# Kernel tuning notes

Hardware: AMD Instinct MI355X
Metric: run time of the kernel (lower is better)

Reference implementation:

```python
import jax, jax.numpy as jnp
import numpy as np

WS = 8      # window_size
NH = 8      # n_heads
EPS = 1e-06


def _rel_coords(ws):
    # Swin-style relative position index table, matches torch buffer construction
    c = np.stack(np.meshgrid(np.arange(ws), np.arange(ws), indexing='ij'))  # [2,ws,ws]
    c = c.reshape(2, -1)                      # [2, L]
    rel = c[:, :, None] - c[:, None, :]       # [2, L, L]
    rel = rel.transpose(1, 2, 0) + (ws - 1)   # [L, L, 2]
    rel[:, :, 0] *= 2 * ws - 1
    return jnp.asarray(rel.sum(-1), dtype=jnp.int32)  # [L, L]


def rms_film(x, t, gw, bw):
    # x: [B,C,H,W], t: [B,d_t]; RMS over channel dim, FiLM scale/shift from t
    g = (t @ gw.T)[:, :, None, None]
    b = (t @ bw.T)[:, :, None, None]
    return g * x * jax.lax.rsqrt(jnp.mean(x * x, axis=1, keepdims=True) + EPS) + b


def window_attn(x, wq, wk, wv, wo_w, wo_b, rpb):
    B, C, H, W = x.shape
    h, w = H // WS, W // WS
    L = WS * WS
    dh = C // NH
    # partition into windows: [B, h, w, L, C]
    xw = x.reshape(B, C, h, WS, w, WS).transpose(0, 2, 4, 3, 5, 1).reshape(B, h, w, L, C)

    def heads(p):
        y = xw @ p.T  # Linear, no bias
        return y.reshape(B, h, w, L, NH, dh).transpose(0, 1, 2, 4, 3, 5)  # [B,h,w,n,L,dh]

    q, k, v = heads(wq), heads(wk), heads(wv)
    bias = rpb[:, _rel_coords(WS)]  # [NH, L, L] gather from bias table
    attn = jnp.einsum('bhwnld,bhwnmd->bhwnlm', q, k) / float(np.sqrt(dh)) + bias
    o = jnp.einsum('bhwnlm,bhwnmd->bhwnld', jax.nn.softmax(attn, axis=-1), v)
    # merge windows, channel order (n c): [B, NH*dh, H, W]
    o = o.reshape(B, h, w, NH, WS, WS, dh).transpose(0, 3, 6, 1, 4, 2, 5).reshape(B, C, H, W)
    # 1x1 conv output projection (with bias)
    return jnp.einsum('bchw,oc->bohw', o, wo_w) + wo_b[None, :, None, None]


def convnext(x, t, dw_w, dw_b, gw, bw, w1, b1, w2, b2):
    # 7x7 depthwise conv, pad 3
    y = jax.lax.conv_general_dilated(
        x, dw_w, window_strides=(1, 1), padding=[(3, 3), (3, 3)],
        dimension_numbers=('NCHW', 'OIHW', 'NCHW'), feature_group_count=x.shape[1])
    y = y + dw_b[None, :, None, None]
    y = rms_film(y, t, gw, bw).transpose(0, 2, 3, 1)  # -> NHWC
    y = jax.nn.gelu(y @ w1.T + b1, approximate=False) @ w2.T + b2
    return y.transpose(0, 3, 1, 2)


def setup_inputs() -> dict:
    key = jax.random.key(0)
    ks = jax.random.split(key, 16)
    D, DT, B, H, W = 256, 256, 8, 128, 128
    DH = 4 * D
    n = lambda k, s: jax.random.normal(k, s, jnp.float32) * 0.02
    return dict(
        x=jax.random.normal(ks[0], (B, D, H, W), jnp.float32),
        t=jax.random.normal(ks[1], (B, DT), jnp.float32),
        an_g=n(ks[2], (D, DT)), an_b=n(ks[3], (D, DT)),
        wq=n(ks[4], (D, D)), wk=n(ks[5], (D, D)), wv=n(ks[6], (D, D)),
        wo_w=n(ks[7], (D, D)), wo_b=jnp.zeros((D,), jnp.float32),
        rpb=n(ks[8], (NH, (2 * WS - 1) ** 2)),
        dw_w=n(ks[9], (D, 1, 7, 7)), dw_b=jnp.zeros((D,), jnp.float32),
        fn_g=n(ks[10], (D, DT)), fn_b=n(ks[11], (D, DT)),
        w1=n(ks[12], (DH, D)), b1=jnp.zeros((DH,), jnp.float32),
        w2=n(ks[13], (D, DH)), b2=jnp.zeros((D,), jnp.float32))


def reference(x, t, an_g, an_b, wq, wk, wv, wo_w, wo_b, rpb,
              dw_w, dw_b, fn_g, fn_b, w1, b1, w2, b2):
    x = x + window_attn(rms_film(x, t, an_g, an_b), wq, wk, wv, wo_w, wo_b, rpb)
    return x + convnext(x, t, dw_w, dw_b, fn_g, fn_b, w1, b1, w2, b2)
```

## Files before the change

### kernel.cpp

```cpp
#include <hip/hip_runtime.h>
#include <math.h>

typedef __attribute__((ext_vector_type(8))) short bf16x8_t;
typedef __attribute__((ext_vector_type(4))) float f32x4;

__device__ __forceinline__ unsigned short f2bf(float f) {
  unsigned int u = __builtin_bit_cast(unsigned int, f);
  u += 0x7FFFu + ((u >> 16) & 1u);
  return (unsigned short)(u >> 16);
}
__device__ __forceinline__ float bf2f(unsigned short h) {
  unsigned int u = ((unsigned int)h) << 16;
  return __builtin_bit_cast(float, u);
}

typedef const __attribute__((address_space(1))) void* as1cv;
typedef __attribute__((address_space(3))) void* as3v;

__device__ __forceinline__ void gld_lds16(const unsigned short* g, unsigned short* l) {
  __builtin_amdgcn_global_load_lds((as1cv)g, (as3v)l, 16, 0, 0);
}

__global__ __launch_bounds__(256) void tvec_kernel(const float* __restrict__ t,
    const float* __restrict__ an_g, const float* __restrict__ an_b,
    const float* __restrict__ fn_g, const float* __restrict__ fn_b,
    float* __restrict__ gvec) {
  int d = threadIdx.x;
  int b = blockIdx.x;
  int m = blockIdx.y;
  __shared__ float ts[256];
  ts[d] = t[b * 256 + d];
  __syncthreads();
  const float* W = (m == 0) ? an_g : (m == 1) ? an_b : (m == 2) ? fn_g : fn_b;
  float acc = 0.f;
  #pragma unroll 8
  for (int k = 0; k < 256; ++k) acc += ts[k] * W[d * 256 + k];
  gvec[(m * 8 + b) * 256 + d] = acc;
}

__global__ __launch_bounds__(256) void wconv_kernel(const float* __restrict__ wq,
    const float* __restrict__ wk, const float* __restrict__ wv, const float* __restrict__ wo,
    const float* __restrict__ w1, const float* __restrict__ w2,
    unsigned short* __restrict__ outp) {
  int i = blockIdx.x * 256 + threadIdx.x;
  const float* src; int off;
  if      (i <  65536) { src = wq; off = 0; }
  else if (i < 131072) { src = wk; off = 65536; }
  else if (i < 196608) { src = wv; off = 131072; }
  else if (i < 262144) { src = wo; off = 196608; }
  else if (i < 524288) { src = w1; off = 262144; }
  else                 { src = w2; off = 524288; }
  outp[i] = f2bf(src[i - off]);
}

template<int IS_BF>
__global__ __launch_bounds__(256) void film_kernel(const void* __restrict__ in_,
    const float* __restrict__ gvec, int gsel, unsigned short* __restrict__ outbf) {
  const float* inf = (const float*)in_;
  const unsigned short* inb = (const unsigned short*)in_;
  int blk = blockIdx.x;
  int b = blk >> 8;
  int p0 = (blk & 255) << 6;
  int lane = threadIdx.x & 63;
  int cg = threadIdx.x >> 6;
  __shared__ unsigned short vals[64][264];
  __shared__ float ssred[4][64];
  __shared__ float rinvs[64];
  size_t base = ((size_t)b << 22) + p0;
  float ss = 0.f;
  #pragma unroll 4
  for (int ci = 0; ci < 64; ++ci) {
    int c = (cg << 6) + ci;
    size_t idx = base + ((size_t)c << 14) + lane;
    float v = IS_BF ? bf2f(inb[idx]) : inf[idx];
    ss += v * v;
    vals[lane][c] = f2bf(v);
  }
  ssred[cg][lane] = ss;
  __syncthreads();
  if (threadIdx.x < 64) {
    float s = ssred[0][threadIdx.x] + ssred[1][threadIdx.x] + ssred[2][threadIdx.x] + ssred[3][threadIdx.x];
    rinvs[threadIdx.x] = rsqrtf(s * (1.0f / 256.0f) + 1e-6f);
  }
  __syncthreads();
  int pix = threadIdx.x >> 2;
  int c0 = (threadIdx.x & 3) << 6;
  float rv = rinvs[pix];
  const float* gp = gvec + ((gsel * 2 + 0) * 8 + b) * 256;
  const float* bp = gvec + ((gsel * 2 + 1) * 8 + b) * 256;
  unsigned short* orow = outbf + (((size_t)b << 14) + p0 + pix) * 256 + c0;
  #pragma unroll
  for (int ch = 0; ch < 8; ++ch) {
    bf16x8_t pack;
    #pragma unroll
    for (int e = 0; e < 8; ++e) {
      int c = c0 + ch * 8 + e;
      float v = bf2f(vals[pix][c]);
      float o = gp[c] * v * rv + bp[c];
      pack[e] = (short)f2bf(o);
    }
    *(bf16x8_t*)(orow + ch * 8) = pack;
  }
}

template<int DO_GELU>
__global__ __launch_bounds__(256) void gemm_kernel(const unsigned short* __restrict__ A,
    const unsigned short* __restrict__ Bw, const float* __restrict__ bias,
    unsigned short* __restrict__ outp, int K, int N) {
  __shared__ unsigned short As[128 * 64];
  __shared__ unsigned short Bs[128 * 64];
  int tid = threadIdx.x;
  int m0 = blockIdx.x << 7;
  int n0 = blockIdx.y << 7;
  int w = tid >> 6, lane = tid & 63;
  int wm = (w >> 1) << 6, wn = (w & 1) << 6;
  f32x4 acc[4][4];
  #pragma unroll
  for (int mi = 0; mi < 4; ++mi)
    #pragma unroll
    for (int ni = 0; ni < 4; ++ni)
      acc[mi][ni] = (f32x4){0.f, 0.f, 0.f, 0.f};

  for (int k0 = 0; k0 < K; k0 += 64) {
    #pragma unroll
    for (int r2 = 0; r2 < 4; ++r2) {
      int linear = (r2 << 8) + tid;
      int row = linear >> 3;
      int ch = linear & 7;
      gld_lds16(A  + (size_t)(m0 + row) * K + k0 + ch * 8, As + linear * 8);
      gld_lds16(Bw + (size_t)(n0 + row) * K + k0 + ch * 8, Bs + linear * 8);
    }
    __syncthreads();
    #pragma unroll
    for (int kk = 0; kk < 64; kk += 32) {
      bf16x8_t af[4], bq[4];
      int lr = lane & 15;
      int lk = ((lane >> 4) << 3) + kk;
      #pragma unroll
      for (int mi = 0; mi < 4; ++mi)
        af[mi] = *(const bf16x8_t*)(As + ((wm + (mi << 4) + lr) << 6) + lk);
      #pragma unroll
      for (int ni = 0; ni < 4; ++ni)
        bq[ni] = *(const bf16x8_t*)(Bs + ((wn + (ni << 4) + lr) << 6) + lk);
      #pragma unroll
      for (int mi = 0; mi < 4; ++mi)
        #pragma unroll
        for (int ni = 0; ni < 4; ++ni)
          acc[mi][ni] = __builtin_amdgcn_mfma_f32_16x16x32_bf16(af[mi], bq[ni], acc[mi][ni], 0, 0, 0);
    }
    __syncthreads();
  }
  int lr = lane & 15, lg = lane >> 4;
  #pragma unroll
  for (int mi = 0; mi < 4; ++mi) {
    #pragma unroll
    for (int ni = 0; ni < 4; ++ni) {
      int col = n0 + wn + (ni << 4) + lr;
      int row = m0 + wm + (mi << 4) + (lg << 2);
      f32x4 a = acc[mi][ni];
      #pragma unroll
      for (int i = 0; i < 4; ++i) {
        float v = a[i];
        if (DO_GELU) {
          v += bias[col];
          v = 0.5f * v * (1.0f + erff(v * 0.70710678118654752f));
        }
        outp[(size_t)(row + i) * N + col] = f2bf(v);
      }
    }
  }
}

__global__ __launch_bounds__(256) void gemm2f_kernel(const unsigned short* __restrict__ A,
    const unsigned short* __restrict__ Bw, const float* __restrict__ bias,
    const unsigned short* __restrict__ x1, float* __restrict__ outp, int m_base) {
  __shared__ unsigned short smem[16384];
  unsigned short* As = smem;
  unsigned short* Bs = smem + 8192;
  const int K = 1024, N = 256;
  int tid = threadIdx.x;
  int m0 = blockIdx.x << 7;
  int n0 = blockIdx.y << 7;
  int w = tid >> 6, lane = tid & 63;
  int wm = (w >> 1) << 6, wn = (w & 1) << 6;
  f32x4 acc[4][4];
  #pragma unroll
  for (int mi = 0; mi < 4; ++mi)
    #pragma unroll
    for (int ni = 0; ni < 4; ++ni)
      acc[mi][ni] = (f32x4){0.f, 0.f, 0.f, 0.f};

  for (int k0 = 0; k0 < K; k0 += 64) {
    #pragma unroll
    for (int r2 = 0; r2 < 4; ++r2) {
      int linear = (r2 << 8) + tid;
      int row = linear >> 3;
      int ch = linear & 7;
      gld_lds16(A  + (size_t)(m0 + row) * K + k0 + ch * 8, As + linear * 8);
      gld_lds16(Bw + (size_t)(n0 + row) * K + k0 + ch * 8, Bs + linear * 8);
    }
    __syncthreads();
    #pragma unroll
    for (int kk = 0; kk < 64; kk += 32) {
      bf16x8_t af[4], bq[4];
      int lr = lane & 15;
      int lk = ((lane >> 4) << 3) + kk;
      #pragma unroll
      for (int mi = 0; mi < 4; ++mi)
        af[mi] = *(const bf16x8_t*)(As + ((wm + (mi << 4) + lr) << 6) + lk);
      #pragma unroll
      for (int ni = 0; ni < 4; ++ni)
        bq[ni] = *(const bf16x8_t*)(Bs + ((wn + (ni << 4) + lr) << 6) + lk);
      #pragma unroll
      for (int mi = 0; mi < 4; ++mi)
        #pragma unroll
        for (int ni = 0; ni < 4; ++ni)
          acc[mi][ni] = __builtin_amdgcn_mfma_f32_16x16x32_bf16(af[mi], bq[ni], acc[mi][ni], 0, 0, 0);
    }
    __syncthreads();
  }

  int lr = lane & 15, lg = lane >> 4;
  #pragma unroll
  for (int mi = 0; mi < 4; ++mi)
    #pragma unroll
    for (int ni = 0; ni < 4; ++ni) {
      int cl = wn + (ni << 4) + lr;
      int rl = wm + (mi << 4) + (lg << 2);
      f32x4 a = acc[mi][ni];
      #pragma unroll
      for (int i = 0; i < 4; ++i)
        smem[cl * 128 + rl + i] = f2bf(a[i]);
    }
  __syncthreads();

  int cl = tid >> 1;
  int half = tid & 1;
  int pglob0 = m_base + m0;
  int b = pglob0 >> 14;
  int pix = (pglob0 & 16383) + half * 64;
  int c = n0 + cl;
  const unsigned short* srow = smem + cl * 128 + half * 64;
  size_t gbase = ((size_t)b * 256 + c) * 16384 + pix;
  const unsigned short* xrow = x1 + gbase;
  float* orow = outp + gbase;
  float bb = bias[c];
  #pragma unroll
  for (int jj = 0; jj < 8; ++jj) {
    bf16x8_t sv = *(const bf16x8_t*)(srow + jj * 8);
    bf16x8_t xv = *(const bf16x8_t*)(xrow + jj * 8);
    #pragma unroll
    for (int e = 0; e < 8; ++e)
      orow[jj * 8 + e] = bf2f((unsigned short)sv[e]) + bf2f((unsigned short)xv[e]) + bb;
  }
}

__global__ __launch_bounds__(256) void attn_kernel(const unsigned short* __restrict__ qg,
    const unsigned short* __restrict__ kg, const unsigned short* __restrict__ vg,
    const float* __restrict__ rpb, unsigned short* __restrict__ og) {
  int wi = blockIdx.x;
  int head = blockIdx.y;
  int b = wi >> 8, wh = (wi >> 4) & 15, ww = wi & 15;
  __shared__ float qs[64][33], ks[64][33], vs[64][33];
  __shared__ float ps[64][65];
  __shared__ float rpbs[225];
  int tid = threadIdx.x;

  {
    int l = tid >> 2, quarter = tid & 3;
    size_t grow = (size_t)b * 16384 + (size_t)(wh * 8 + (l >> 3)) * 128 + ww * 8 + (l & 7);
    size_t goff = grow * 256 + head * 32 + quarter * 8;
    bf16x8_t qv = *(const bf16x8_t*)(qg + goff);
    bf16x8_t kv = *(const bf16x8_t*)(kg + goff);
    bf16x8_t vv = *(const bf16x8_t*)(vg + goff);
    #pragma unroll
    for (int e = 0; e < 8; ++e) {
      qs[l][quarter * 8 + e] = bf2f((unsigned short)qv[e]);
      ks[l][quarter * 8 + e] = bf2f((unsigned short)kv[e]);
      vs[l][quarter * 8 + e] = bf2f((unsigned short)vv[e]);
    }
  }
  if (tid < 225) rpbs[tid] = rpb[head * 225 + tid];
  __syncthreads();

  int r0 = (tid >> 4) * 4, c0 = (tid & 15) * 4;
  float s[4][4] = {};
  for (int k = 0; k < 32; ++k) {
    float qa[4], kb[4];
    #pragma unroll
    for (int i = 0; i < 4; ++i) { qa[i] = qs[r0 + i][k]; kb[i] = ks[c0 + i][k]; }
    #pragma unroll
    for (int i = 0; i < 4; ++i)
      #pragma unroll
      for (int j = 0; j < 4; ++j) s[i][j] += qa[i] * kb[j];
  }
  const float scale = 0.17677669529663689f;
  float sum[4];
  #pragma unroll
  for (int i = 0; i < 4; ++i) {
    int row = r0 + i; int il = row >> 3, jl = row & 7;
    #pragma unroll
    for (int j = 0; j < 4; ++j) {
      int col = c0 + j; int im = col >> 3, jm = col & 7;
      s[i][j] = s[i][j] * scale + rpbs[(il - im + 7) * 15 + (jl - jm + 7)];
    }
    float mx = fmaxf(fmaxf(s[i][0], s[i][1]), fmaxf(s[i][2], s[i][3]));
    mx = fmaxf(mx, __shfl_xor(mx, 1));
    mx = fmaxf(mx, __shfl_xor(mx, 2));
    mx = fmaxf(mx, __shfl_xor(mx, 4));
    mx = fmaxf(mx, __shfl_xor(mx, 8));
    float sm = 0.f;
    #pragma unroll
    for (int j = 0; j < 4; ++j) { s[i][j] = __expf(s[i][j] - mx); sm += s[i][j]; }
    sm += __shfl_xor(sm, 1);
    sm += __shfl_xor(sm, 2);
    sm += __shfl_xor(sm, 4);
    sm += __shfl_xor(sm, 8);
    sum[i] = sm;
    #pragma unroll
    for (int j = 0; j < 4; ++j) ps[row][c0 + j] = s[i][j];
  }
  __syncthreads();

  int d0 = (tid & 15) * 2;
  float o[4][2] = {};
  for (int m = 0; m < 64; ++m) {
    float pa[4], vb0 = vs[m][d0], vb1 = vs[m][d0 + 1];
    #pragma unroll
    for (int i = 0; i < 4; ++i) pa[i] = ps[r0 + i][m];
    #pragma unroll
    for (int i = 0; i < 4; ++i) { o[i][0] += pa[i] * vb0; o[i][1] += pa[i] * vb1; }
  }
  #pragma unroll
  for (int i = 0; i < 4; ++i) {
    int row = r0 + i;
    size_t orow = ((size_t)b * 16384 + (size_t)(wh * 8 + (row >> 3)) * 128 + ww * 8 + (row & 7)) * 256 + head * 32;
    float inv = 1.0f / sum[i];
    unsigned int packed = (unsigned int)f2bf(o[i][0] * inv) | ((unsigned int)f2bf(o[i][1] * inv) << 16);
    *(unsigned int*)(og + orow + d0) = packed;
  }
}

__global__ __launch_bounds__(256) void addt1_kernel(const unsigned short* __restrict__ src,
    const float* __restrict__ resid, const float* __restrict__ bias,
    unsigned short* __restrict__ outp) {
  int blk = blockIdx.x;
  int b = blk >> 8;
  int p0 = (blk & 255) << 6;
  __shared__ unsigned short vals[64][264];
  int tid = threadIdx.x;
  #pragma unroll
  for (int r = 0; r < 8; ++r) {
    int linear = r * 256 + tid;
    int row = linear >> 5;
    int ch = linear & 31;
    bf16x8_t v = *(const bf16x8_t*)(src + (((size_t)b << 14) + p0 + row) * 256 + ch * 8);
    *(bf16x8_t*)(&vals[row][ch * 8]) = v;
  }
  __syncthreads();
  int lane = tid & 63;
  int cq = tid >> 6;
  #pragma unroll 4
  for (int ci = 0; ci < 64; ++ci) {
    int c = (cq << 6) + ci;
    float v = bf2f(vals[lane][c]);
    size_t gidx = ((size_t)b << 22) + ((size_t)c << 14) + p0 + lane;
    outp[gidx] = f2bf(resid[gidx] + v + bias[c]);
  }
}

__global__ __launch_bounds__(256) void dwconv_kernel(const unsigned short* __restrict__ x1,
    const float* __restrict__ w, const float* __restrict__ bias, unsigned short* __restrict__ outp) {
  int bc = blockIdx.y;
  int c = bc & 255;
  int y0 = blockIdx.x << 6;
  __shared__ unsigned short tile[70 * 144];
  __shared__ float wf[49];
  const unsigned short* plane = x1 + ((size_t)bc << 14);
  int tid = threadIdx.x;

  for (int idx = tid; idx < 70 * 16; idx += 256) {
    int row = idx >> 4, ch = idx & 15;
    int gy = y0 - 3 + row;
    bf16x8_t v = (bf16x8_t){0, 0, 0, 0, 0, 0, 0, 0};
    if (gy >= 0 && gy < 128) v = *(const bf16x8_t*)(plane + gy * 128 + ch * 8);
    *(bf16x8_t*)(&tile[row * 144 + 8 + ch * 8]) = v;
  }
  for (int idx = tid; idx < 70 * 6; idx += 256) {
    int row = idx / 6, e = idx % 6;
    int col = (e < 3) ? (5 + e) : (133 + e);
    tile[row * 144 + col] = 0;
  }
  if (tid < 49) wf[tid] = w[c * 49 + tid];
  __syncthreads();

  int r = tid >> 2;
  int c0 = (tid & 3) << 5;
  float acc[32];
  float bb = bias[c];
  #pragma unroll
  for (int i = 0; i < 32; ++i) acc[i] = bb;

  #pragma unroll
  for (int u = 0; u < 7; ++u) {
    const unsigned short* rowp = &tile[(r + u) * 144 + c0];
    float f[48];
    #pragma unroll
    for (int k = 0; k < 6; ++k) {
      bf16x8_t v = *(const bf16x8_t*)(rowp + k * 8);
      #pragma unroll
      for (int e = 0; e < 8; ++e) f[k * 8 + e] = bf2f((unsigned short)v[e]);
    }
    #pragma unroll
    for (int t = 0; t < 7; ++t) {
      float wv = wf[u * 7 + t];
      #pragma unroll
      for (int i = 0; i < 32; ++i) acc[i] += f[i + 5 + t] * wv;
    }
  }

  unsigned short* orow = outp + ((size_t)bc << 14) + (size_t)(y0 + r) * 128 + c0;
  #pragma unroll
  for (int k = 0; k < 4; ++k) {
    bf16x8_t v;
    #pragma unroll
    for (int e = 0; e < 8; ++e) v[e] = (short)f2bf(acc[k * 8 + e]);
    *(bf16x8_t*)(orow + k * 8) = v;
  }
}

extern "C" void kernel_launch(void* const* d_in, const int* in_sizes, int n_in,
                              void* d_out, int out_size, void* d_ws, size_t ws_size,
                              hipStream_t stream) {
  const float* x    = (const float*)d_in[0];
  const float* t    = (const float*)d_in[1];
  const float* an_g = (const float*)d_in[2];
  const float* an_b = (const float*)d_in[3];
  const float* wq   = (const float*)d_in[4];
  const float* wk   = (const float*)d_in[5];
  const float* wv   = (const float*)d_in[6];
  const float* wo_w = (const float*)d_in[7];
  const float* wo_b = (const float*)d_in[8];
  const float* rpb  = (const float*)d_in[9];
  const float* dw_w = (const float*)d_in[10];
  const float* dw_b = (const float*)d_in[11];
  const float* fn_g = (const float*)d_in[12];
  const float* fn_b = (const float*)d_in[13];
  const float* w1   = (const float*)d_in[14];
  const float* b1   = (const float*)d_in[15];
  const float* w2   = (const float*)d_in[16];
  const float* b2   = (const float*)d_in[17];
  float* outp = (float*)d_out;

  char* ws = (char*)d_ws;
  const size_t MB = 1024ull * 1024ull;
  float* gvec = (float*)ws;
  unsigned short* wbf = (unsigned short*)(ws + 32768);
  unsigned short* P = (unsigned short*)(ws + 2 * MB);
  unsigned short* Q = (unsigned short*)(ws + 66 * MB);
  unsigned short* R = (unsigned short*)(ws + 130 * MB);
  unsigned short* vbuf = (unsigned short*)((char*)d_out + 64 * MB);

  unsigned short* wq_bf = wbf;
  unsigned short* wk_bf = wbf + 65536;
  unsigned short* wv_bf = wbf + 131072;
  unsigned short* wo_bf = wbf + 196608;
  unsigned short* w1_bf = wbf + 262144;
  unsigned short* w2_bf = wbf + 524288;

  tvec_kernel<<<dim3(8, 4), 256, 0, stream>>>(t, an_g, an_b, fn_g, fn_b, gvec);
  wconv_kernel<<<3072, 256, 0, stream>>>(wq, wk, wv, wo_w, w1, w2, wbf);

  film_kernel<0><<<2048, 256, 0, stream>>>(x, gvec, 0, P);

  gemm_kernel<0><<<dim3(1024, 2), 256, 0, stream>>>(P, wq_bf, nullptr, Q, 256, 256);
  gemm_kernel<0><<<dim3(1024, 2), 256, 0, stream>>>(P, wk_bf, nullptr, R, 256, 256);
  gemm_kernel<0><<<dim3(1024, 2), 256, 0, stream>>>(P, wv_bf, nullptr, vbuf, 256, 256);

  attn_kernel<<<dim3(2048, 8), 256, 0, stream>>>(Q, R, vbuf, rpb, P);

  gemm_kernel<0><<<dim3(1024, 2), 256, 0, stream>>>(P, wo_bf, nullptr, Q, 256, 256);
  addt1_kernel<<<2048, 256, 0, stream>>>(Q, x, wo_b, R);

  dwconv_kernel<<<dim3(2, 2048), 256, 0, stream>>>(R, dw_w, dw_b, Q);
  film_kernel<1><<<2048, 256, 0, stream>>>(Q, gvec, 1, P);

  for (int qtr = 0; qtr < 4; ++qtr) {
    int m_base = qtr * 32768;
    gemm_kernel<1><<<dim3(256, 8), 256, 0, stream>>>(P + (size_t)m_base * 256, w1_bf, b1, Q, 256, 1024);
    gemm2f_kernel<<<dim3(256, 2), 256, 0, stream>>>(Q, w2_bf, b2, R, outp, m_base);
  }
}
```

Measured before the change: 1.020 ms.

## Rewrite window attention with bf16 MFMA and channel-major V projection

Window attention now runs both QK^T and PV on bf16 MFMA instructions instead of scalar fp32 FMAs from LDS. Each block handles one window for all 8 heads, with each wave covering two heads. A new GEMM variant writes V transposed (channel-major) so that PV B-fragments load directly from global memory. Softmax probabilities are rounded to bf16 before the PV product, which adds a small precision loss, and the shared-memory footprint changes with a launch-bounds occupancy hint.

```diff
diff --git a/kernel.cpp b/kernel.cpp
--- a/kernel.cpp
+++ b/kernel.cpp
@@ -171,6 +171,80 @@
   }
 }
 
+__global__ __launch_bounds__(256) void gemm_t_kernel(const unsigned short* __restrict__ A,
+    const unsigned short* __restrict__ Bw, unsigned short* __restrict__ outp) {
+  __shared__ unsigned short smem[16384];
+  unsigned short* As = smem;
+  unsigned short* Bs = smem + 8192;
+  const int K = 256;
+  int tid = threadIdx.x;
+  int m0 = blockIdx.x << 7;
+  int n0 = blockIdx.y << 7;
+  int w = tid >> 6, lane = tid & 63;
+  int wm = (w >> 1) << 6, wn = (w & 1) << 6;
+  f32x4 acc[4][4];
+  #pragma unroll
+  for (int mi = 0; mi < 4; ++mi)
+    #pragma unroll
+    for (int ni = 0; ni < 4; ++ni)
+      acc[mi][ni] = (f32x4){0.f, 0.f, 0.f, 0.f};
+
+  for (int k0 = 0; k0 < K; k0 += 64) {
+    #pragma unroll
+    for (int r2 = 0; r2 < 4; ++r2) {
+      int linear = (r2 << 8) + tid;
+      int row = linear >> 3;
+      int ch = linear & 7;
+      gld_lds16(A  + (size_t)(m0 + row) * K + k0 + ch * 8, As + linear * 8);
+      gld_lds16(Bw + (size_t)(n0 + row) * K + k0 + ch * 8, Bs + linear * 8);
+    }
+    __syncthreads();
+    #pragma unroll
+    for (int kk = 0; kk < 64; kk += 32) {
+      bf16x8_t af[4], bq[4];
+      int lr = lane & 15;
+      int lk = ((lane >> 4) << 3) + kk;
+      #pragma unroll
+      for (int mi = 0; mi < 4; ++mi)
+        af[mi] = *(const bf16x8_t*)(As + ((wm + (mi << 4) + lr) << 6) + lk);
+      #pragma unroll
+      for (int ni = 0; ni < 4; ++ni)
+        bq[ni] = *(const bf16x8_t*)(Bs + ((wn + (ni << 4) + lr) << 6) + lk);
+      #pragma unroll
+      for (int mi = 0; mi < 4; ++mi)
+        #pragma unroll
+        for (int ni = 0; ni < 4; ++ni)
+          acc[mi][ni] = __builtin_amdgcn_mfma_f32_16x16x32_bf16(af[mi], bq[ni], acc[mi][ni], 0, 0, 0);
+    }
+    __syncthreads();
+  }
+
+  int lr = lane & 15, lg = lane >> 4;
+  #pragma unroll
+  for (int mi = 0; mi < 4; ++mi)
+    #pragma unroll
+    for (int ni = 0; ni < 4; ++ni) {
+      int cl = wn + (ni << 4) + lr;
+      int rl = wm + (mi << 4) + (lg << 2);
+      f32x4 a = acc[mi][ni];
+      #pragma unroll
+      for (int i = 0; i < 4; ++i)
+        smem[cl * 128 + rl + i] = f2bf(a[i]);
+    }
+  __syncthreads();
+
+  int cl = tid >> 1;
+  int half = tid & 1;
+  int b = m0 >> 14;
+  int pix = (m0 & 16383) + half * 64;
+  int c = n0 + cl;
+  const unsigned short* srow = smem + cl * 128 + half * 64;
+  unsigned short* orow = outp + ((size_t)b * 256 + c) * 16384 + pix;
+  #pragma unroll
+  for (int jj = 0; jj < 8; ++jj)
+    *(bf16x8_t*)(orow + jj * 8) = *(const bf16x8_t*)(srow + jj * 8);
+}
+
 __global__ __launch_bounds__(256) void gemm2f_kernel(const unsigned short* __restrict__ A,
     const unsigned short* __restrict__ Bw, const float* __restrict__ bias,
     const unsigned short* __restrict__ x1, float* __restrict__ outp, int m_base) {
@@ -255,89 +329,110 @@
   }
 }
 
-__global__ __launch_bounds__(256) void attn_kernel(const unsigned short* __restrict__ qg,
-    const unsigned short* __restrict__ kg, const unsigned short* __restrict__ vg,
+__global__ __launch_bounds__(256, 3) void attn_kernel(const unsigned short* __restrict__ qg,
+    const unsigned short* __restrict__ kg, const unsigned short* __restrict__ vt,
     const float* __restrict__ rpb, unsigned short* __restrict__ og) {
+  __shared__ float rpbf[1800];
+  __shared__ unsigned short pbuf[4][64 * 72];
   int wi = blockIdx.x;
-  int head = blockIdx.y;
   int b = wi >> 8, wh = (wi >> 4) & 15, ww = wi & 15;
-  __shared__ float qs[64][33], ks[64][33], vs[64][33];
-  __shared__ float ps[64][65];
-  __shared__ float rpbs[225];
   int tid = threadIdx.x;
-
-  {
-    int l = tid >> 2, quarter = tid & 3;
-    size_t grow = (size_t)b * 16384 + (size_t)(wh * 8 + (l >> 3)) * 128 + ww * 8 + (l & 7);
-    size_t goff = grow * 256 + head * 32 + quarter * 8;
-    bf16x8_t qv = *(const bf16x8_t*)(qg + goff);
-    bf16x8_t kv = *(const bf16x8_t*)(kg + goff);
-    bf16x8_t vv = *(const bf16x8_t*)(vg + goff);
-    #pragma unroll
-    for (int e = 0; e < 8; ++e) {
-      qs[l][quarter * 8 + e] = bf2f((unsigned short)qv[e]);
-      ks[l][quarter * 8 + e] = bf2f((unsigned short)kv[e]);
-      vs[l][quarter * 8 + e] = bf2f((unsigned short)vv[e]);
-    }
-  }
-  if (tid < 225) rpbs[tid] = rpb[head * 225 + tid];
-  __syncthreads();
-
-  int r0 = (tid >> 4) * 4, c0 = (tid & 15) * 4;
-  float s[4][4] = {};
-  for (int k = 0; k < 32; ++k) {
-    float qa[4], kb[4];
-    #pragma unroll
-    for (int i = 0; i < 4; ++i) { qa[i] = qs[r0 + i][k]; kb[i] = ks[c0 + i][k]; }
-    #pragma unroll
-    for (int i = 0; i < 4; ++i)
-      #pragma unroll
-      for (int j = 0; j < 4; ++j) s[i][j] += qa[i] * kb[j];
-  }
+  int w = tid >> 6, lane = tid & 63;
+  int g = lane >> 4, lr = lane & 15;
+  for (int idx = tid; idx < 1800; idx += 256) rpbf[idx] = rpb[idx];
+  __syncthreads();
+
+  int rowpix = (wh * 8) * 128 + ww * 8;
+  size_t ibase = ((size_t)b << 14) + rowpix;
+  unsigned short* pb = pbuf[w];
   const float scale = 0.17677669529663689f;
-  float sum[4];
-  #pragma unroll
-  for (int i = 0; i < 4; ++i) {
-    int row = r0 + i; int il = row >> 3, jl = row & 7;
-    #pragma unroll
-    for (int j = 0; j < 4; ++j) {
-      int col = c0 + j; int im = col >> 3, jm = col & 7;
-      s[i][j] = s[i][j] * scale + rpbs[(il - im + 7) * 15 + (jl - jm + 7)];
-    }
-    float mx = fmaxf(fmaxf(s[i][0], s[i][1]), fmaxf(s[i][2], s[i][3]));
-    mx = fmaxf(mx, __shfl_xor(mx, 1));
-    mx = fmaxf(mx, __shfl_xor(mx, 2));
-    mx = fmaxf(mx, __shfl_xor(mx, 4));
-    mx = fmaxf(mx, __shfl_xor(mx, 8));
-    float sm = 0.f;
-    #pragma unroll
-    for (int j = 0; j < 4; ++j) { s[i][j] = __expf(s[i][j] - mx); sm += s[i][j]; }
-    sm += __shfl_xor(sm, 1);
-    sm += __shfl_xor(sm, 2);
-    sm += __shfl_xor(sm, 4);
-    sm += __shfl_xor(sm, 8);
-    sum[i] = sm;
-    #pragma unroll
-    for (int j = 0; j < 4; ++j) ps[row][c0 + j] = s[i][j];
-  }
-  __syncthreads();
-
-  int d0 = (tid & 15) * 2;
-  float o[4][2] = {};
-  for (int m = 0; m < 64; ++m) {
-    float pa[4], vb0 = vs[m][d0], vb1 = vs[m][d0 + 1];
-    #pragma unroll
-    for (int i = 0; i < 4; ++i) pa[i] = ps[r0 + i][m];
-    #pragma unroll
-    for (int i = 0; i < 4; ++i) { o[i][0] += pa[i] * vb0; o[i][1] += pa[i] * vb1; }
-  }
-  #pragma unroll
-  for (int i = 0; i < 4; ++i) {
-    int row = r0 + i;
-    size_t orow = ((size_t)b * 16384 + (size_t)(wh * 8 + (row >> 3)) * 128 + ww * 8 + (row & 7)) * 256 + head * 32;
-    float inv = 1.0f / sum[i];
-    unsigned int packed = (unsigned int)f2bf(o[i][0] * inv) | ((unsigned int)f2bf(o[i][1] * inv) << 16);
-    *(unsigned int*)(og + orow + d0) = packed;
+
+  #pragma unroll 1
+  for (int hh = 0; hh < 2; ++hh) {
+    int h = w * 2 + hh;
+    float sums[4][4];
+    {
+      bf16x8_t qf[4], kf[4];
+      #pragma unroll
+      for (int t = 0; t < 4; ++t) {
+        size_t tok = ibase + (size_t)(t * 2 + (lr >> 3)) * 128 + (lr & 7);
+        qf[t] = *(const bf16x8_t*)(qg + tok * 256 + h * 32 + g * 8);
+        kf[t] = *(const bf16x8_t*)(kg + tok * 256 + h * 32 + g * 8);
+      }
+      f32x4 sacc[4][4];
+      #pragma unroll
+      for (int qt = 0; qt < 4; ++qt)
+        #pragma unroll
+        for (int kt = 0; kt < 4; ++kt)
+          sacc[qt][kt] = __builtin_amdgcn_mfma_f32_16x16x32_bf16(qf[qt], kf[kt],
+                           (f32x4){0.f, 0.f, 0.f, 0.f}, 0, 0, 0);
+      const float* rb = &rpbf[h * 225];
+      #pragma unroll
+      for (int qt = 0; qt < 4; ++qt) {
+        #pragma unroll
+        for (int i = 0; i < 4; ++i) {
+          int q = qt * 16 + g * 4 + i;
+          int il = q >> 3, jl = q & 7;
+          float v[4];
+          #pragma unroll
+          for (int kt = 0; kt < 4; ++kt) {
+            int kv = kt * 16 + lr;
+            v[kt] = sacc[qt][kt][i] * scale + rb[(il - (kv >> 3) + 7) * 15 + (jl - (kv & 7) + 7)];
+          }
+          float mx = fmaxf(fmaxf(v[0], v[1]), fmaxf(v[2], v[3]));
+          mx = fmaxf(mx, __shfl_xor(mx, 1));
+          mx = fmaxf(mx, __shfl_xor(mx, 2));
+          mx = fmaxf(mx, __shfl_xor(mx, 4));
+          mx = fmaxf(mx, __shfl_xor(mx, 8));
+          float sm = 0.f;
+          #pragma unroll
+          for (int kt = 0; kt < 4; ++kt) { v[kt] = __expf(v[kt] - mx); sm += v[kt]; }
+          sm += __shfl_xor(sm, 1);
+          sm += __shfl_xor(sm, 2);
+          sm += __shfl_xor(sm, 4);
+          sm += __shfl_xor(sm, 8);
+          sums[qt][i] = sm;
+          #pragma unroll
+          for (int kt = 0; kt < 4; ++kt)
+            pb[q * 72 + kt * 16 + lr] = f2bf(v[kt]);
+        }
+      }
+    }
+    f32x4 oacc[4][2];
+    #pragma unroll
+    for (int qt = 0; qt < 4; ++qt) {
+      oacc[qt][0] = (f32x4){0.f, 0.f, 0.f, 0.f};
+      oacc[qt][1] = (f32x4){0.f, 0.f, 0.f, 0.f};
+    }
+    #pragma unroll
+    for (int ks = 0; ks < 2; ++ks) {
+      bf16x8_t pf[4], vf[2];
+      #pragma unroll
+      for (int qt = 0; qt < 4; ++qt)
+        pf[qt] = *(const bf16x8_t*)(pb + (qt * 16 + lr) * 72 + ks * 32 + g * 8);
+      #pragma unroll
+      for (int dt = 0; dt < 2; ++dt) {
+        size_t plane = (size_t)b * 256 + h * 32 + dt * 16 + lr;
+        vf[dt] = *(const bf16x8_t*)(vt + (plane << 14) + rowpix + (size_t)(ks * 4 + g) * 128);
+      }
+      #pragma unroll
+      for (int qt = 0; qt < 4; ++qt)
+        #pragma unroll
+        for (int dt = 0; dt < 2; ++dt)
+          oacc[qt][dt] = __builtin_amdgcn_mfma_f32_16x16x32_bf16(pf[qt], vf[dt], oacc[qt][dt], 0, 0, 0);
+    }
+    #pragma unroll
+    for (int qt = 0; qt < 4; ++qt) {
+      #pragma unroll
+      for (int i = 0; i < 4; ++i) {
+        int q = qt * 16 + g * 4 + i;
+        float inv = 1.0f / sums[qt][i];
+        size_t tok = ibase + (size_t)(q >> 3) * 128 + (q & 7);
+        #pragma unroll
+        for (int dt = 0; dt < 2; ++dt)
+          og[tok * 256 + h * 32 + dt * 16 + lr] = f2bf(oacc[qt][dt][i] * inv);
+      }
+    }
   }
 }
 
@@ -475,9 +570,9 @@
 
   gemm_kernel<0><<<dim3(1024, 2), 256, 0, stream>>>(P, wq_bf, nullptr, Q, 256, 256);
   gemm_kernel<0><<<dim3(1024, 2), 256, 0, stream>>>(P, wk_bf, nullptr, R, 256, 256);
-  gemm_kernel<0><<<dim3(1024, 2), 256, 0, stream>>>(P, wv_bf, nullptr, vbuf, 256, 256);
-
-  attn_kernel<<<dim3(2048, 8), 256, 0, stream>>>(Q, R, vbuf, rpb, P);
+  gemm_t_kernel<<<dim3(1024, 2), 256, 0, stream>>>(P, wv_bf, vbuf);
+
+  attn_kernel<<<2048, 256, 0, stream>>>(Q, R, vbuf, rpb, P);
 
   gemm_kernel<0><<<dim3(1024, 2), 256, 0, stream>>>(P, wo_bf, nullptr, Q, 256, 256);
   addt1_kernel<<<2048, 256, 0, stream>>>(Q, x, wo_b, R);
```

After: 958.1 us. -6.1%, faster.
